# Performance work log

Hardware: AMD Instinct MI355X
Metric: run time of the kernel (lower is better)

The kernel has to match this reference:

```python
import jax, jax.numpy as jnp
import numpy as np

Q_HEADS, KV_HEADS, HEAD_SIZE, H, MAX_LEN = 16, 4, 64, 1024, 4096
B, S = 1, 4096


def _rope_tables(max_len, head_size):
    half = head_size // 2
    inv_freq = 1.0 / (10000.0 ** (np.arange(half, dtype=np.float32) / half))
    pos = np.arange(max_len, dtype=np.float32)
    ang = pos[:, None] * inv_freq[None, :]  # [max_len, half]
    return jnp.asarray(np.sin(ang)), jnp.asarray(np.cos(ang))


def setup_inputs() -> dict:
    key = jax.random.key(0)
    ks = jax.random.split(key, 6)
    sc = 1.0 / np.sqrt(H)
    x = jax.random.normal(ks[0], (B, S, H), dtype=jnp.float32)
    wq = jax.random.normal(ks[1], (H, H), dtype=jnp.float32) * sc
    wk = jax.random.normal(ks[2], (H, KV_HEADS * HEAD_SIZE), dtype=jnp.float32) * sc
    wv = jax.random.normal(ks[3], (H, KV_HEADS * HEAD_SIZE), dtype=jnp.float32) * sc
    wo = jax.random.normal(ks[4], (H, H), dtype=jnp.float32) * sc
    sin, cos = _rope_tables(MAX_LEN, HEAD_SIZE)
    full_mask = jnp.tril(jnp.ones((MAX_LEN, MAX_LEN), dtype=bool))
    attention_mask = jnp.ones((B, S), dtype=jnp.int32)
    return {"x": x, "attention_mask": attention_mask, "start": 0,
            "wq": wq, "wk": wk, "wv": wv, "wo": wo,
            "sin": sin, "cos": cos, "full_mask": full_mask}


def _rotate(t, sin, cos, start):
    # t: [b, heads, s, head_size]; interleaved even/odd RoPE
    s = t.shape[2]
    sn = sin[start:start + s, :][None, None, :, :]
    cs = cos[start:start + s, :][None, None, :, :]
    even, odd = t[..., 0::2], t[..., 1::2]
    out_even = cs * even - sn * odd
    out_odd = sn * even + cs * odd
    return jnp.stack((out_even, out_odd), axis=-1).reshape(t.shape)


def _expand_kv(t, group):
    # [b, kv_heads, s, d] -> [b, kv_heads*group, s, d]
    b, kvh, s, d = t.shape
    return jnp.broadcast_to(t[:, :, None], (b, kvh, group, s, d)).reshape(b, kvh * group, s, d)


def reference(x, attention_mask, start, wq, wk, wv, wo, sin, cos, full_mask):
    b, s, _ = x.shape
    group = Q_HEADS // KV_HEADS
    Q = (x @ wq).reshape(b, s, Q_HEADS, HEAD_SIZE).transpose(0, 2, 1, 3)
    K = (x @ wk).reshape(b, s, KV_HEADS, HEAD_SIZE).transpose(0, 2, 1, 3)
    V = (x @ wv).reshape(b, s, KV_HEADS, HEAD_SIZE).transpose(0, 2, 1, 3)
    Q = _rotate(Q, sin, cos, start)
    K = _rotate(K, sin, cos, start)
    K = _expand_kv(K, group)
    V = _expand_kv(V, group)
    z = jnp.einsum('bhqd,bhkd->bhqk', Q, K) / (HEAD_SIZE ** 0.5)
    kv_len = start + s
    mask = full_mask[:s, :kv_len][None, None, :, :]
    amask = (attention_mask[:, :kv_len] != 0)[:, None, None, :]
    mask = mask & amask
    z = jnp.where(mask, z, -1000000.0)
    A = jax.nn.softmax(z, axis=-1)
    ctx = jnp.einsum('bhqk,bhkd->bhqd', A, V)
    q_mask = attention_mask[:, :s].astype(ctx.dtype)[:, None, :, None]
    ctx = ctx * q_mask
    ctx = ctx.transpose(0, 2, 1, 3).reshape(b, s, H)
    return ctx @ wo
```

## Files before the change

### kernel.cpp

```cpp
#include <hip/hip_runtime.h>

typedef __bf16 bf16x8 __attribute__((ext_vector_type(8)));
typedef float f32x4 __attribute__((ext_vector_type(4)));
typedef unsigned int u32x4 __attribute__((ext_vector_type(4)));

typedef const void __attribute__((address_space(1)))* gas1;
typedef void __attribute__((address_space(3)))* las3;

__device__ __forceinline__ unsigned short f2bf(float f) {
  unsigned int u = __builtin_bit_cast(unsigned int, f);
  u += 0x7fffu + ((u >> 16) & 1u);
  return (unsigned short)(u >> 16);
}
__device__ __forceinline__ float bf2f(unsigned short h) {
  unsigned int u = ((unsigned int)h) << 16;
  return __builtin_bit_cast(float, u);
}
__device__ __forceinline__ unsigned int pack2bf(float lo, float hi) {
  return (unsigned int)f2bf(lo) | ((unsigned int)f2bf(hi) << 16);
}
__device__ __forceinline__ unsigned int packtr(float lo, float hi) {
  return __builtin_amdgcn_perm(__builtin_bit_cast(unsigned int, hi),
                               __builtin_bit_cast(unsigned int, lo), 0x07060302u);
}

__global__ __launch_bounds__(256) void prep(const float* __restrict__ x,
                                            const float* __restrict__ wq,
                                            const float* __restrict__ wk,
                                            const float* __restrict__ wv,
                                            const float* __restrict__ wo,
                                            const float* __restrict__ sinT,
                                            const float* __restrict__ cosT,
                                            unsigned short* __restrict__ xb,
                                            unsigned short* __restrict__ wtqkv,
                                            unsigned short* __restrict__ wot,
                                            float2* __restrict__ scT) {
  __shared__ float tile[32][33];
  const int b = blockIdx.x;
  const int tid = threadIdx.x;
  if (b < 4096) {
    int i = b * 256 + tid;
    float4 v = ((const float4*)x)[i];
    uint2 o;
    o.x = pack2bf(v.x, v.y);
    o.y = pack2bf(v.z, v.w);
    ((uint2*)xb)[i] = o;
    return;
  }
  if (b >= 6656) {
    int idx = (b - 6656) * 256 + tid;
    scT[idx] = make_float2(sinT[idx], cosT[idx]);
    return;
  }
  const float* src;
  unsigned short* dst;
  int R, C, t;
  if (b < 5120)      { t = b - 4096; src = wq; dst = wtqkv;               R = 1024; C = 1024; }
  else if (b < 5376) { t = b - 5120; src = wk; dst = wtqkv + 1024 * 1024; R = 1024; C = 256; }
  else if (b < 5632) { t = b - 5376; src = wv; dst = wtqkv + 1280 * 1024; R = 1024; C = 256; }
  else               { t = b - 5632; src = wo; dst = wot;                 R = 1024; C = 1024; }
  const int ntc = C >> 5;
  const int c0 = (t % ntc) * 32, r0 = (t / ntc) * 32;
  const int tx = tid & 31, ty = tid >> 5;
#pragma unroll
  for (int i = 0; i < 4; ++i)
    tile[ty + i * 8][tx] = src[(r0 + ty + i * 8) * C + c0 + tx];
  __syncthreads();
#pragma unroll
  for (int i = 0; i < 4; ++i)
    dst[(c0 + ty + i * 8) * R + r0 + tx] = f2bf(tile[tx][ty + i * 8]);
}

__global__ __launch_bounds__(64, 4) void gemm_qkv(const unsigned short* __restrict__ A,
                                                  const unsigned short* __restrict__ Bt,
                                                  const float2* __restrict__ scT,
                                                  unsigned short* __restrict__ Qh,
                                                  unsigned short* __restrict__ Kh,
                                                  unsigned short* __restrict__ Vt) {
  __shared__ __align__(16) unsigned short Als[64 * 32];
  __shared__ __align__(16) unsigned short Bls[64 * 32];
  const int K = 1024;
  const int lane = threadIdx.x;
  const int lgrp = lane >> 4, lmod = lane & 15;
  const int m0 = blockIdx.y * 64, n0 = blockIdx.x * 64;
  const int lr = lane >> 2, lc = (lane & 3) * 8;

  f32x4 acc[4][4] = {};

  for (int k0 = 0; k0 < K; k0 += 32) {
    __syncthreads();
#pragma unroll
    for (int i = 0; i < 4; ++i) {
      __builtin_amdgcn_global_load_lds((gas1)(const void*)&A[(size_t)(m0 + i * 16 + lr) * K + k0 + lc],
                                       (las3)(void*)&Als[i * 512], 16, 0, 0);
      __builtin_amdgcn_global_load_lds((gas1)(const void*)&Bt[(size_t)(n0 + i * 16 + lr) * K + k0 + lc],
                                       (las3)(void*)&Bls[i * 512], 16, 0, 0);
    }
    __syncthreads();
    bf16x8 af[4], bfr[4];
#pragma unroll
    for (int mi = 0; mi < 4; ++mi)
      af[mi] = __builtin_bit_cast(bf16x8, *(const u32x4*)&Als[(mi * 16 + lmod) * 32 + lgrp * 8]);
#pragma unroll
    for (int ni = 0; ni < 4; ++ni)
      bfr[ni] = __builtin_bit_cast(bf16x8, *(const u32x4*)&Bls[(ni * 16 + lmod) * 32 + lgrp * 8]);
#pragma unroll
    for (int mi = 0; mi < 4; ++mi)
#pragma unroll
      for (int ni = 0; ni < 4; ++ni)
        acc[mi][ni] = __builtin_amdgcn_mfma_f32_16x16x32_bf16(af[mi], bfr[ni], acc[mi][ni], 0, 0, 0);
  }

  if (n0 >= 1280) {
    const int kvh = (n0 - 1280) >> 6;
#pragma unroll
    for (int mi = 0; mi < 4; ++mi)
#pragma unroll
      for (int ni = 0; ni < 4; ++ni) {
        int d = ni * 16 + lmod;
        int s = m0 + mi * 16 + lgrp * 4;
        uint2 o;
        o.x = pack2bf(acc[mi][ni][0], acc[mi][ni][1]);
        o.y = pack2bf(acc[mi][ni][2], acc[mi][ni][3]);
        *(uint2*)&Vt[((size_t)(kvh * 64 + d)) * 4096 + s] = o;
      }
    return;
  }

  const float qscale = 0.18033688011112042f;
  const bool isQ = (n0 < 1024);
  const int h = isQ ? (n0 >> 6) : ((n0 - 1024) >> 6);
  unsigned short* dstbase = isQ ? Qh : Kh;
  const bool evn = (lmod & 1) == 0;
#pragma unroll
  for (int mi = 0; mi < 4; ++mi)
#pragma unroll
    for (int ni = 0; ni < 4; ++ni) {
      int d = ni * 16 + lmod;
      int i = d >> 1;
#pragma unroll
      for (int r = 0; r < 4; ++r) {
        float v = acc[mi][ni][r];
        float pp = __shfl_xor(v, 1, 64);
        int rl = mi * 16 + lgrp * 4 + r;
        float2 sc = scT[(size_t)(m0 + rl) * 32 + i];
        float e = evn ? v : pp, o = evn ? pp : v;
        float outv = evn ? (sc.y * e - sc.x * o) : (sc.x * e + sc.y * o);
        if (isQ) outv *= qscale;
        dstbase[((size_t)h * 4096 + m0 + rl) * 64 + d] = f2bf(outv);
      }
    }
}

__global__ __launch_bounds__(64, 4) void gemm_out(const unsigned short* __restrict__ A,
                                                  const unsigned short* __restrict__ Bt,
                                                  float* __restrict__ Cout) {
  __shared__ __align__(16) unsigned short Als[64 * 32];
  __shared__ __align__(16) unsigned short Bls[64 * 32];
  const int K = 1024, N = 1024;
  const int lane = threadIdx.x;
  const int lgrp = lane >> 4, lmod = lane & 15;
  const int m0 = blockIdx.y * 64, n0 = blockIdx.x * 64;
  const int lr = lane >> 2, lc = (lane & 3) * 8;

  f32x4 acc[4][4] = {};

  for (int k0 = 0; k0 < K; k0 += 32) {
    __syncthreads();
#pragma unroll
    for (int i = 0; i < 4; ++i) {
      __builtin_amdgcn_global_load_lds((gas1)(const void*)&A[(size_t)(m0 + i * 16 + lr) * K + k0 + lc],
                                       (las3)(void*)&Als[i * 512], 16, 0, 0);
      __builtin_amdgcn_global_load_lds((gas1)(const void*)&Bt[(size_t)(n0 + i * 16 + lr) * K + k0 + lc],
                                       (las3)(void*)&Bls[i * 512], 16, 0, 0);
    }
    __syncthreads();
    bf16x8 af[4], bfr[4];
#pragma unroll
    for (int mi = 0; mi < 4; ++mi)
      af[mi] = __builtin_bit_cast(bf16x8, *(const u32x4*)&Als[(mi * 16 + lmod) * 32 + lgrp * 8]);
#pragma unroll
    for (int ni = 0; ni < 4; ++ni)
      bfr[ni] = __builtin_bit_cast(bf16x8, *(const u32x4*)&Bls[(ni * 16 + lmod) * 32 + lgrp * 8]);
#pragma unroll
    for (int mi = 0; mi < 4; ++mi)
#pragma unroll
      for (int ni = 0; ni < 4; ++ni)
        acc[mi][ni] = __builtin_amdgcn_mfma_f32_16x16x32_bf16(af[mi], bfr[ni], acc[mi][ni], 0, 0, 0);
  }

#pragma unroll
  for (int mi = 0; mi < 4; ++mi)
#pragma unroll
    for (int ni = 0; ni < 4; ++ni)
#pragma unroll
      for (int r = 0; r < 4; ++r) {
        int row = m0 + mi * 16 + lgrp * 4 + r;
        int col = n0 + ni * 16 + lmod;
        Cout[(size_t)row * N + col] = acc[mi][ni][r];
      }
}

__global__ __launch_bounds__(256, 2) void attn3(const unsigned short* __restrict__ Qh,
                                                const unsigned short* __restrict__ Kh,
                                                const unsigned short* __restrict__ Vt,
                                                unsigned short* __restrict__ ctx) {
  __shared__ __align__(16) unsigned short Kls[128 * 68];
  __shared__ __align__(16) unsigned short Vls[64 * 136];
  const int bx = blockIdx.x;
  const int head = bx & 15;
  const int qidx = bx >> 4;
  const int qb = (qidx < 16) ? (31 - qidx) : (qidx - 16);
  const int kvh = head >> 2;
  const int tid = threadIdx.x;
  const int wave = tid >> 6, lane = tid & 63;
  const int lgrp = lane >> 4, lmod = lane & 15;
  const int qbase = qb * 128;

  const unsigned short* Kg = Kh + (size_t)kvh * 4096 * 64;
  const unsigned short* Vg = Vt + (size_t)kvh * 64 * 4096;

  bf16x8 qf[2][2];
  int qrow[2];
#pragma unroll
  for (int qt = 0; qt < 2; ++qt) {
    qrow[qt] = qbase + wave * 32 + qt * 16 + lmod;
    const unsigned short* Qg = Qh + ((size_t)head * 4096 + qrow[qt]) * 64;
    qf[qt][0] = __builtin_bit_cast(bf16x8, *(const u32x4*)&Qg[lgrp * 8]);
    qf[qt][1] = __builtin_bit_cast(bf16x8, *(const u32x4*)&Qg[32 + lgrp * 8]);
  }

  const int kbase = (8 * (lmod >> 2) + (lmod & 3)) * 68 + lgrp * 8;
  const int vbase = lmod * 136 + lgrp * 8;

  f32x4 accO[2][4] = {};
  float m_i[2] = {-3e38f, -3e38f}, l_i[2] = {0.f, 0.f};

  for (int kc = 0; kc <= qb; ++kc) {
    const int kb = kc * 128;
    __syncthreads();
#pragma unroll
    for (int i = 0; i < 4; ++i) {
      int ii = tid + i * 256;
      int r = ii >> 3, sg = (ii & 7) * 8;
      u32x4 dK = *(const u32x4*)&Kg[(size_t)(kb + r) * 64 + sg];
      uint2* pd = (uint2*)&Kls[r * 68 + sg];
      pd[0] = make_uint2(dK[0], dK[1]);
      pd[1] = make_uint2(dK[2], dK[3]);
    }
#pragma unroll
    for (int i = 0; i < 4; ++i) {
      int ii = tid + i * 256;
      int r = ii >> 4, sg = (ii & 15) * 8;
      *(u32x4*)&Vls[r * 136 + sg] = *(const u32x4*)&Vg[(size_t)r * 4096 + kb + sg];
    }
    __syncthreads();

    f32x4 s[4][2][2];
#pragma unroll
    for (int g = 0; g < 4; ++g)
#pragma unroll
      for (int t = 0; t < 2; ++t) {
        const unsigned short* ka = &Kls[kbase + (32 * g + 4 * t) * 68];
        uint2 a0 = *(const uint2*)&ka[0];
        uint2 a1 = *(const uint2*)&ka[4];
        uint2 b0 = *(const uint2*)&ka[32];
        uint2 b1 = *(const uint2*)&ka[36];
        u32x4 lo = {a0.x, a0.y, a1.x, a1.y};
        u32x4 hi = {b0.x, b0.y, b1.x, b1.y};
        bf16x8 alo = __builtin_bit_cast(bf16x8, lo);
        bf16x8 ahi = __builtin_bit_cast(bf16x8, hi);
#pragma unroll
        for (int qt = 0; qt < 2; ++qt) {
          f32x4 z = {};
          z = __builtin_amdgcn_mfma_f32_16x16x32_bf16(alo, qf[qt][0], z, 0, 0, 0);
          z = __builtin_amdgcn_mfma_f32_16x16x32_bf16(ahi, qf[qt][1], z, 0, 0, 0);
          s[g][t][qt] = z;
        }
      }

#pragma unroll
    for (int qt = 0; qt < 2; ++qt) {
      if (kb + 127 > qbase + wave * 32 + qt * 16) {
#pragma unroll
        for (int g = 0; g < 4; ++g)
#pragma unroll
          for (int t = 0; t < 2; ++t)
#pragma unroll
            for (int r = 0; r < 4; ++r) {
              int key = kb + 32 * g + 8 * lgrp + 4 * t + r;
              if (key > qrow[qt]) s[g][t][qt][r] = -3e38f;
            }
      }
    }

#pragma unroll
    for (int qt = 0; qt < 2; ++qt) {
      f32x4 v0 = s[0][0][qt], v1 = s[0][1][qt];
#pragma unroll
      for (int g = 1; g < 4; ++g)
#pragma unroll
        for (int r = 0; r < 4; ++r) {
          v0[r] = fmaxf(v0[r], s[g][0][qt][r]);
          v1[r] = fmaxf(v1[r], s[g][1][qt][r]);
        }
      float mx = fmaxf(fmaxf(fmaxf(v0[0], v0[1]), fmaxf(v0[2], v0[3])),
                       fmaxf(fmaxf(v1[0], v1[1]), fmaxf(v1[2], v1[3])));
      mx = fmaxf(mx, __shfl_xor(mx, 16, 64));
      mx = fmaxf(mx, __shfl_xor(mx, 32, 64));
      float mnew = fmaxf(m_i[qt], mx);
      float alpha = __builtin_amdgcn_exp2f(m_i[qt] - mnew);
      m_i[qt] = mnew;
      f32x4 su = {};
#pragma unroll
      for (int g = 0; g < 4; ++g)
#pragma unroll
        for (int t = 0; t < 2; ++t)
#pragma unroll
          for (int r = 0; r < 4; ++r) {
            float ev = __builtin_amdgcn_exp2f(s[g][t][qt][r] - mnew);
            s[g][t][qt][r] = ev;
            su[r] += ev;
          }
      float rs = (su[0] + su[1]) + (su[2] + su[3]);
      rs += __shfl_xor(rs, 16, 64);
      rs += __shfl_xor(rs, 32, 64);
      l_i[qt] = l_i[qt] * alpha + rs;
#pragma unroll
      for (int dt = 0; dt < 4; ++dt)
#pragma unroll
        for (int r = 0; r < 4; ++r) accO[qt][dt][r] *= alpha;
    }

#pragma unroll
    for (int g = 0; g < 4; ++g) {
      bf16x8 pf[2];
#pragma unroll
      for (int qt = 0; qt < 2; ++qt) {
        u32x4 pk;
        pk[0] = packtr(s[g][0][qt][0], s[g][0][qt][1]);
        pk[1] = packtr(s[g][0][qt][2], s[g][0][qt][3]);
        pk[2] = packtr(s[g][1][qt][0], s[g][1][qt][1]);
        pk[3] = packtr(s[g][1][qt][2], s[g][1][qt][3]);
        pf[qt] = __builtin_bit_cast(bf16x8, pk);
      }
#pragma unroll
      for (int dt = 0; dt < 4; ++dt) {
        bf16x8 vf = __builtin_bit_cast(bf16x8, *(const u32x4*)&Vls[vbase + dt * 2176 + 32 * g]);
        accO[0][dt] = __builtin_amdgcn_mfma_f32_16x16x32_bf16(vf, pf[0], accO[0][dt], 0, 0, 0);
        accO[1][dt] = __builtin_amdgcn_mfma_f32_16x16x32_bf16(vf, pf[1], accO[1][dt], 0, 0, 0);
      }
    }
  }

#pragma unroll
  for (int qt = 0; qt < 2; ++qt) {
    float inv = 1.f / l_i[qt];
#pragma unroll
    for (int dt = 0; dt < 4; ++dt) {
      uint2 o;
      o.x = pack2bf(accO[qt][dt][0] * inv, accO[qt][dt][1] * inv);
      o.y = pack2bf(accO[qt][dt][2] * inv, accO[qt][dt][3] * inv);
      *(uint2*)&ctx[(size_t)qrow[qt] * 1024 + head * 64 + dt * 16 + lgrp * 4] = o;
    }
  }
}

extern "C" void kernel_launch(void* const* d_in, const int* in_sizes, int n_in,
                              void* d_out, int out_size, void* d_ws, size_t ws_size,
                              hipStream_t stream) {
  const float* x    = (const float*)d_in[0];
  const float* wq   = (const float*)d_in[3];
  const float* wk   = (const float*)d_in[4];
  const float* wv   = (const float*)d_in[5];
  const float* wo   = (const float*)d_in[6];
  const float* sinT = (const float*)d_in[7];
  const float* cosT = (const float*)d_in[8];

  unsigned short* ws    = (unsigned short*)d_ws;
  unsigned short* xb    = ws;
  unsigned short* wtqkv = xb + 4096 * 1024;
  unsigned short* wot   = wtqkv + 1536 * 1024;
  unsigned short* Qh    = wot + 1024 * 1024;
  unsigned short* Kh    = Qh + 16 * 4096 * 64;
  unsigned short* Vt    = Kh + 4 * 4096 * 64;
  unsigned short* ctx   = Vt + 4 * 64 * 4096;
  float2* scT           = (float2*)(ctx + 4096 * 1024);
  float* out = (float*)d_out;

  prep<<<7168, 256, 0, stream>>>(x, wq, wk, wv, wo, sinT, cosT, xb, wtqkv, wot, scT);
  gemm_qkv<<<dim3(24, 64), 64, 0, stream>>>(xb, wtqkv, scT, Qh, Kh, Vt);
  attn3<<<dim3(512), 256, 0, stream>>>(Qh, Kh, Vt, ctx);
  gemm_out<<<dim3(16, 64), 64, 0, stream>>>(ctx, wot, out);
}
```

Before: 248.8 us.

## Rewrite QKV and output GEMMs with 128x128 tiles, double-buffered swizzled LDS

```diff
diff --git a/kernel.cpp b/kernel.cpp
--- a/kernel.cpp
+++ b/kernel.cpp
@@ -71,54 +71,97 @@
     dst[(c0 + ty + i * 8) * R + r0 + tx] = f2bf(tile[tx][ty + i * 8]);
 }
 
-__global__ __launch_bounds__(64, 4) void gemm_qkv(const unsigned short* __restrict__ A,
-                                                  const unsigned short* __restrict__ Bt,
-                                                  const float2* __restrict__ scT,
-                                                  unsigned short* __restrict__ Qh,
-                                                  unsigned short* __restrict__ Kh,
-                                                  unsigned short* __restrict__ Vt) {
-  __shared__ __align__(16) unsigned short Als[64 * 32];
-  __shared__ __align__(16) unsigned short Bls[64 * 32];
-  const int K = 1024;
-  const int lane = threadIdx.x;
+
+__device__ __forceinline__ void stage_tile(const unsigned short* __restrict__ src,
+                                           unsigned short* lds, int tid) {
+  const int w = tid >> 6;
+  const int l = tid & 63;
+  const int rsub = l >> 3;
+  const int cblk = l & 7;
+#pragma unroll
+  for (int i = 0; i < 4; ++i) {
+    const int row = i * 32 + w * 8 + rsub;
+    const int scol = (cblk ^ (row & 7)) * 8;
+    __builtin_amdgcn_global_load_lds((gas1)(const void*)&src[(size_t)row * 1024 + scol],
+                                     (las3)(void*)&lds[(i * 32 + w * 8) * 64], 16, 0, 0);
+  }
+}
+
+#define GEMM_STEP(CUR, NXT, KNEXT, DO_STAGE)                                          \
+  {                                                                                   \
+    if (DO_STAGE) {                                                                   \
+      stage_tile(Ab + (KNEXT), sm[NXT][0], tid);                                      \
+      stage_tile(Bb + (KNEXT), sm[NXT][1], tid);                                      \
+    }                                                                                 \
+    const char* As = (const char*)sm[CUR][0];                                         \
+    const char* Bs = (const char*)sm[CUR][1];                                         \
+    bf16x8 af[2][4], bfr[2][4];                                                       \
+    _Pragma("unroll")                                                                 \
+    for (int kk = 0; kk < 2; ++kk) {                                                  \
+      const int co = (kk * 64 + lgrp * 16) ^ xorsel;                                  \
+      _Pragma("unroll")                                                               \
+      for (int mi = 0; mi < 4; ++mi)                                                  \
+        af[kk][mi] = __builtin_bit_cast(bf16x8,                                       \
+            *(const u32x4*)(As + arow + mi * 2048 + co));                             \
+      _Pragma("unroll")                                                               \
+      for (int ni = 0; ni < 4; ++ni)                                                  \
+        bfr[kk][ni] = __builtin_bit_cast(bf16x8,                                      \
+            *(const u32x4*)(Bs + brow + ni * 2048 + co));                             \
+    }                                                                                 \
+    _Pragma("unroll")                                                                 \
+    for (int kk = 0; kk < 2; ++kk)                                                    \
+      _Pragma("unroll")                                                               \
+      for (int mi = 0; mi < 4; ++mi)                                                  \
+        _Pragma("unroll")                                                             \
+        for (int ni = 0; ni < 4; ++ni)                                                \
+          acc[mi][ni] = __builtin_amdgcn_mfma_f32_16x16x32_bf16(af[kk][mi],           \
+                            bfr[kk][ni], acc[mi][ni], 0, 0, 0);                       \
+    __syncthreads();                                                                  \
+  }
+
+__global__ __launch_bounds__(256, 2) void gemm_qkv(const unsigned short* __restrict__ A,
+                                                   const unsigned short* __restrict__ Bt,
+                                                   const float2* __restrict__ scT,
+                                                   unsigned short* __restrict__ Qh,
+                                                   unsigned short* __restrict__ Kh,
+                                                   unsigned short* __restrict__ Vt) {
+  __shared__ __align__(16) unsigned short sm[2][2][128 * 64];
+  const int tid = threadIdx.x;
+  const int bid = blockIdx.x;
+  const int swz = (bid & 7) * 48 + (bid >> 3);
+  const int nt = swz % 12, mt = swz / 12;
+  const int m0 = mt * 128, n0 = nt * 128;
+
+  const int lane = tid & 63, wid = tid >> 6;
+  const int wr = wid >> 1, wc = wid & 1;
   const int lgrp = lane >> 4, lmod = lane & 15;
-  const int m0 = blockIdx.y * 64, n0 = blockIdx.x * 64;
-  const int lr = lane >> 2, lc = (lane & 3) * 8;
+  const int xorsel = (lmod & 7) << 4;
+  const int arow = (wr * 64 + lmod) * 128;
+  const int brow = (wc * 64 + lmod) * 128;
+
+  const unsigned short* Ab = A + (size_t)m0 * 1024;
+  const unsigned short* Bb = Bt + (size_t)n0 * 1024;
 
   f32x4 acc[4][4] = {};
 
-  for (int k0 = 0; k0 < K; k0 += 32) {
-    __syncthreads();
-#pragma unroll
-    for (int i = 0; i < 4; ++i) {
-      __builtin_amdgcn_global_load_lds((gas1)(const void*)&A[(size_t)(m0 + i * 16 + lr) * K + k0 + lc],
-                                       (las3)(void*)&Als[i * 512], 16, 0, 0);
-      __builtin_amdgcn_global_load_lds((gas1)(const void*)&Bt[(size_t)(n0 + i * 16 + lr) * K + k0 + lc],
-                                       (las3)(void*)&Bls[i * 512], 16, 0, 0);
-    }
-    __syncthreads();
-    bf16x8 af[4], bfr[4];
-#pragma unroll
-    for (int mi = 0; mi < 4; ++mi)
-      af[mi] = __builtin_bit_cast(bf16x8, *(const u32x4*)&Als[(mi * 16 + lmod) * 32 + lgrp * 8]);
-#pragma unroll
-    for (int ni = 0; ni < 4; ++ni)
-      bfr[ni] = __builtin_bit_cast(bf16x8, *(const u32x4*)&Bls[(ni * 16 + lmod) * 32 + lgrp * 8]);
-#pragma unroll
-    for (int mi = 0; mi < 4; ++mi)
-#pragma unroll
-      for (int ni = 0; ni < 4; ++ni)
-        acc[mi][ni] = __builtin_amdgcn_mfma_f32_16x16x32_bf16(af[mi], bfr[ni], acc[mi][ni], 0, 0, 0);
-  }
-
-  if (n0 >= 1280) {
-    const int kvh = (n0 - 1280) >> 6;
+  stage_tile(Ab, sm[0][0], tid);
+  stage_tile(Bb, sm[0][1], tid);
+  __syncthreads();
+
+  for (int t = 0; t < 16; t += 2) {
+    GEMM_STEP(0, 1, (size_t)(t + 1) * 64, true);
+    GEMM_STEP(1, 0, (size_t)(t + 2) * 64, t < 14);
+  }
+
+  const int ncol0 = n0 + wc * 64;
+  if (ncol0 >= 1280) {
+    const int kvh = (ncol0 - 1280) >> 6;
 #pragma unroll
     for (int mi = 0; mi < 4; ++mi)
 #pragma unroll
       for (int ni = 0; ni < 4; ++ni) {
         int d = ni * 16 + lmod;
-        int s = m0 + mi * 16 + lgrp * 4;
+        int s = m0 + wr * 64 + mi * 16 + lgrp * 4;
         uint2 o;
         o.x = pack2bf(acc[mi][ni][0], acc[mi][ni][1]);
         o.y = pack2bf(acc[mi][ni][2], acc[mi][ni][3]);
@@ -128,8 +171,8 @@
   }
 
   const float qscale = 0.18033688011112042f;
-  const bool isQ = (n0 < 1024);
-  const int h = isQ ? (n0 >> 6) : ((n0 - 1024) >> 6);
+  const bool isQ = (ncol0 < 1024);
+  const int h = isQ ? (ncol0 >> 6) : ((ncol0 - 1024) >> 6);
   unsigned short* dstbase = isQ ? Qh : Kh;
   const bool evn = (lmod & 1) == 0;
 #pragma unroll
@@ -142,62 +185,56 @@
       for (int r = 0; r < 4; ++r) {
         float v = acc[mi][ni][r];
         float pp = __shfl_xor(v, 1, 64);
-        int rl = mi * 16 + lgrp * 4 + r;
-        float2 sc = scT[(size_t)(m0 + rl) * 32 + i];
+        int row = m0 + wr * 64 + mi * 16 + lgrp * 4 + r;
+        float2 sc = scT[(size_t)row * 32 + i];
         float e = evn ? v : pp, o = evn ? pp : v;
         float outv = evn ? (sc.y * e - sc.x * o) : (sc.x * e + sc.y * o);
         if (isQ) outv *= qscale;
-        dstbase[((size_t)h * 4096 + m0 + rl) * 64 + d] = f2bf(outv);
-      }
-    }
-}
-
-__global__ __launch_bounds__(64, 4) void gemm_out(const unsigned short* __restrict__ A,
-                                                  const unsigned short* __restrict__ Bt,
-                                                  float* __restrict__ Cout) {
-  __shared__ __align__(16) unsigned short Als[64 * 32];
-  __shared__ __align__(16) unsigned short Bls[64 * 32];
-  const int K = 1024, N = 1024;
-  const int lane = threadIdx.x;
+        dstbase[((size_t)h * 4096 + row) * 64 + d] = f2bf(outv);
+      }
+    }
+}
+
+__global__ __launch_bounds__(256, 2) void gemm_out(const unsigned short* __restrict__ A,
+                                                   const unsigned short* __restrict__ Bt,
+                                                   float* __restrict__ Cout) {
+  __shared__ __align__(16) unsigned short sm[2][2][128 * 64];
+  const int tid = threadIdx.x;
+  const int bid = blockIdx.x;
+  const int swz = (bid & 7) * 32 + (bid >> 3);
+  const int nt = swz & 7, mt = swz >> 3;
+  const int m0 = mt * 128, n0 = nt * 128;
+
+  const int lane = tid & 63, wid = tid >> 6;
+  const int wr = wid >> 1, wc = wid & 1;
   const int lgrp = lane >> 4, lmod = lane & 15;
-  const int m0 = blockIdx.y * 64, n0 = blockIdx.x * 64;
-  const int lr = lane >> 2, lc = (lane & 3) * 8;
+  const int xorsel = (lmod & 7) << 4;
+  const int arow = (wr * 64 + lmod) * 128;
+  const int brow = (wc * 64 + lmod) * 128;
+
+  const unsigned short* Ab = A + (size_t)m0 * 1024;
+  const unsigned short* Bb = Bt + (size_t)n0 * 1024;
 
   f32x4 acc[4][4] = {};
 
-  for (int k0 = 0; k0 < K; k0 += 32) {
-    __syncthreads();
-#pragma unroll
-    for (int i = 0; i < 4; ++i) {
-      __builtin_amdgcn_global_load_lds((gas1)(const void*)&A[(size_t)(m0 + i * 16 + lr) * K + k0 + lc],
-                                       (las3)(void*)&Als[i * 512], 16, 0, 0);
-      __builtin_amdgcn_global_load_lds((gas1)(const void*)&Bt[(size_t)(n0 + i * 16 + lr) * K + k0 + lc],
-                                       (las3)(void*)&Bls[i * 512], 16, 0, 0);
-    }
-    __syncthreads();
-    bf16x8 af[4], bfr[4];
-#pragma unroll
-    for (int mi = 0; mi < 4; ++mi)
-      af[mi] = __builtin_bit_cast(bf16x8, *(const u32x4*)&Als[(mi * 16 + lmod) * 32 + lgrp * 8]);
+  stage_tile(Ab, sm[0][0], tid);
+  stage_tile(Bb, sm[0][1], tid);
+  __syncthreads();
+
+  for (int t = 0; t < 16; t += 2) {
+    GEMM_STEP(0, 1, (size_t)(t + 1) * 64, true);
+    GEMM_STEP(1, 0, (size_t)(t + 2) * 64, t < 14);
+  }
+
+#pragma unroll
+  for (int mi = 0; mi < 4; ++mi)
 #pragma unroll
     for (int ni = 0; ni < 4; ++ni)
-      bfr[ni] = __builtin_bit_cast(bf16x8, *(const u32x4*)&Bls[(ni * 16 + lmod) * 32 + lgrp * 8]);
-#pragma unroll
-    for (int mi = 0; mi < 4; ++mi)
-#pragma unroll
-      for (int ni = 0; ni < 4; ++ni)
-        acc[mi][ni] = __builtin_amdgcn_mfma_f32_16x16x32_bf16(af[mi], bfr[ni], acc[mi][ni], 0, 0, 0);
-  }
-
-#pragma unroll
-  for (int mi = 0; mi < 4; ++mi)
-#pragma unroll
-    for (int ni = 0; ni < 4; ++ni)
 #pragma unroll
       for (int r = 0; r < 4; ++r) {
-        int row = m0 + mi * 16 + lgrp * 4 + r;
-        int col = n0 + ni * 16 + lmod;
-        Cout[(size_t)row * N + col] = acc[mi][ni][r];
+        int row = m0 + wr * 64 + mi * 16 + lgrp * 4 + r;
+        int col = n0 + wc * 64 + ni * 16 + lmod;
+        Cout[(size_t)row * 1024 + col] = acc[mi][ni][r];
       }
 }
 
@@ -389,7 +426,7 @@
   float* out = (float*)d_out;
 
   prep<<<7168, 256, 0, stream>>>(x, wq, wk, wv, wo, sinT, cosT, xb, wtqkv, wot, scT);
-  gemm_qkv<<<dim3(24, 64), 64, 0, stream>>>(xb, wtqkv, scT, Qh, Kh, Vt);
+  gemm_qkv<<<384, 256, 0, stream>>>(xb, wtqkv, scT, Qh, Kh, Vt);
   attn3<<<dim3(512), 256, 0, stream>>>(Qh, Kh, Vt, ctx);
-  gemm_out<<<dim3(16, 64), 64, 0, stream>>>(ctx, wot, out);
-}
+  gemm_out<<<256, 256, 0, stream>>>(ctx, wot, out);
+}
```

Measured after the change: 232.9 us. 6.4% less time.
